# Kernel tuning notes

Hardware: AMD Instinct MI355X
Metric: run time of the kernel (lower is better)

The kernel has to match this reference:

```python
import jax, jax.numpy as jnp
import numpy as np
from jax import lax

ATT = 16
SK = 3
LK = 13
CIN = 64
RED = 2


def setup_inputs() -> dict:
    key = jax.random.key(0)
    ks = jax.random.split(key, 8)
    B, C, H, W = 16, CIN, 192, 192
    hid = ATT // RED
    x = jax.random.normal(ks[0], (B, C, H, W), dtype=jnp.float32)
    # kernel_gen: 1x1 convs on pooled features -> represented as dense matrices
    w1 = jax.random.normal(ks[1], (hid, ATT), dtype=jnp.float32) * (1.0 / np.sqrt(ATT))
    b1 = jnp.zeros((hid,), dtype=jnp.float32)
    # torch init zeros these; use small random values so the branch is exercised
    w2 = jax.random.normal(ks[2], (ATT * SK * SK, hid), dtype=jnp.float32) * 0.02
    b2 = jax.random.normal(ks[3], (ATT * SK * SK,), dtype=jnp.float32) * 0.02
    # kaiming fan_out for relu: std = sqrt(2 / (out_c * k * k))
    lk_std = np.sqrt(2.0 / (ATT * LK * LK))
    lk_filter = jax.random.normal(ks[4], (ATT, ATT, LK, LK), dtype=jnp.float32) * lk_std
    fusion_w = jax.random.normal(ks[5], (CIN, CIN), dtype=jnp.float32) * (1.0 / np.sqrt(CIN))
    fusion_b = jax.random.normal(ks[6], (CIN,), dtype=jnp.float32) * 0.01
    return {"x": x, "w1": w1, "b1": b1, "w2": w2, "b2": b2,
            "lk_filter": lk_filter, "fusion_w": fusion_w, "fusion_b": fusion_b}


def _forward(x, w1, b1, w2, b2, lk_filter, fusion_w, fusion_b):
    B, C, H, W = x.shape
    F_att, F_idt = x[:, :ATT], x[:, ATT:]

    # kernel_gen: global avg pool -> 1x1 conv -> GELU (exact) -> 1x1 conv
    pooled = F_att.mean(axis=(2, 3))                       # (B, ATT)
    h1 = jax.nn.gelu(pooled @ w1.T + b1, approximate=False)  # (B, ATT//RED)
    k = (h1 @ w2.T + b2).reshape(B, ATT, SK, SK)           # per-sample depthwise kernels

    # dynamic per-sample depthwise conv: 9-tap shifted multiply-accumulate
    pad = SK // 2
    xp = jnp.pad(F_att, ((0, 0), (0, 0), (pad, pad), (pad, pad)))
    out_dk = jnp.zeros_like(F_att)
    for i in range(SK):
        for j in range(SK):
            out_dk = out_dk + xp[:, :, i:i + H, j:j + W] * k[:, :, i, j][:, :, None, None]

    # dense large-kernel conv, padding 'same'
    lp = LK // 2
    out_lk = lax.conv_general_dilated(
        F_att, lk_filter, window_strides=(1, 1),
        padding=((lp, lp), (lp, lp)),
        dimension_numbers=("NCHW", "OIHW", "NCHW"))

    out = jnp.concatenate([out_lk + out_dk, F_idt], axis=1)  # (B, CIN, H, W)
    # fusion 1x1 conv
    out = jnp.einsum("bchw,oc->bohw", out, fusion_w) + fusion_b[None, :, None, None]
    return out


def reference(x, w1, b1, w2, b2, lk_filter, fusion_w, fusion_b):
    return _forward(x, w1, b1, w2, b2, lk_filter, fusion_w, fusion_b)
```

## Files before the change

kernel.cpp:

```cpp
#include <hip/hip_runtime.h>
#include <math.h>

#define ATT 16
#define SKK 3
#define LKK 13
#define CIN 64
#define HID 8
#define BB 16
#define HH 192
#define WW 192
#define HW (HH*WW)
#define NTAP 178
#define NPAIR 89

#define TH 16
#define TW 32
#define TILE_H (TH+12)
#define TILE_W (TW+12)
#define TILE_PX (TILE_H*TILE_W)
#define HSZ (TILE_PX*16)

#define FSTRIDE 144

typedef __attribute__((ext_vector_type(8))) short short8;
typedef __attribute__((ext_vector_type(4))) float f32x4;

__device__ inline unsigned short f2bf(float f) {
    unsigned u = __builtin_bit_cast(unsigned, f);
    unsigned r = u + 0x7FFFu + ((u >> 16) & 1u);
    return (unsigned short)(r >> 16);
}

__global__ __launch_bounds__(256) void pool_kernel(const float* __restrict__ x,
                                                   float* __restrict__ pooled) {
    int bc = blockIdx.x;
    int b = bc >> 4, c = bc & 15;
    const float4* p = (const float4*)(x + ((size_t)(b*CIN + c)) * HW);
    float s = 0.f;
    #pragma unroll 4
    for (int i = threadIdx.x; i < (HW/4); i += 256) {
        float4 v = p[i];
        s += (v.x + v.y) + (v.z + v.w);
    }
    #pragma unroll
    for (int off = 32; off > 0; off >>= 1) s += __shfl_down(s, off, 64);
    __shared__ float red[4];
    int lane = threadIdx.x & 63, wid = threadIdx.x >> 6;
    if (lane == 0) red[wid] = s;
    __syncthreads();
    if (threadIdx.x == 0)
        pooled[bc] = (red[0] + red[1] + red[2] + red[3]) * (1.0f/HW);
}

__global__ __launch_bounds__(256) void mlp_kernel(const float* __restrict__ pooled,
                                                  const float* __restrict__ w1,
                                                  const float* __restrict__ b1,
                                                  const float* __restrict__ w2,
                                                  const float* __restrict__ b2,
                                                  float* __restrict__ kout) {
    __shared__ float h1[BB][HID];
    int t = threadIdx.x;
    if (t < BB*HID) {
        int b = t / HID, j = t % HID;
        float s = b1[j];
        #pragma unroll
        for (int a = 0; a < ATT; ++a) s += pooled[b*ATT + a] * w1[j*ATT + a];
        h1[b][j] = 0.5f * s * (1.0f + erff(s * 0.70710678118654752440f));
    }
    __syncthreads();
    for (int idx = t; idx < BB*ATT*SKK*SKK; idx += 256) {
        int b = idx / (ATT*SKK*SKK), o = idx % (ATT*SKK*SKK);
        float s = b2[o];
        #pragma unroll
        for (int a = 0; a < HID; ++a) s += h1[b][a] * w2[o*HID + a];
        kout[idx] = s;
    }
}

__global__ __launch_bounds__(256) void build_kernel(const float* __restrict__ lk,
                                                    const float* __restrict__ kdyn,
                                                    const float* __restrict__ fw,
                                                    unsigned short* __restrict__ wB,
                                                    unsigned short* __restrict__ fwBt) {
    int idx = blockIdx.x*256 + threadIdx.x;
    const int total = BB*NTAP*256;
    if (idx < total) {
        int b   = idx / (NTAP*256);
        int rem = idx % (NTAP*256);
        int t   = rem >> 8;
        int co  = (rem >> 4) & 15;
        int ci  = rem & 15;
        float v;
        if (t < 169) v = lk[(co*ATT + ci)*169 + t];
        else { int d = t - 169; v = (ci == co) ? kdyn[(b*ATT + ci)*9 + d] : 0.f; }
        wB[idx] = f2bf(v);
    } else {
        int j = idx - total;
        if (j < CIN*CIN) fwBt[j] = f2bf(fw[j]);
    }
}

__global__ __launch_bounds__(256, 3) void conv_mfma_kernel(const float* __restrict__ x,
                                                           const unsigned short* __restrict__ wB,
                                                           float* __restrict__ convres) {
    __shared__ char ldsA[2*HSZ];
    __shared__ int  lut[NTAP];
    const int b    = blockIdx.y;
    const int tile = blockIdx.x;
    const int h0   = (tile / (WW/TW)) * TH;
    const int w0   = (tile % (WW/TW)) * TW;
    const int tid  = threadIdx.x;

    if (tid < NTAP) {
        int off;
        if (tid < 169) off = (tid/13)*TILE_W + (tid%13);
        else { int d = tid - 169; off = (5 + d/3)*TILE_W + (5 + d%3); }
        lut[tid] = off * 16;
    }

    const float* xb = x + (size_t)b*CIN*HW;
    #pragma unroll
    for (int c4 = 0; c4 < 8; ++c4) {
        const float* p0 = xb + (size_t)(2*c4)*HW;
        const float* p1 = p0 + HW;
        const int half = c4 >> 2, c2 = c4 & 3;
        for (int base = 0; base < TILE_PX; base += 256) {
            int px = base + tid;
            if (px < TILE_PX) {
                int tr = px / TILE_W, tc = px % TILE_W;
                int gh = h0 + tr - 6, gw = w0 + tc - 6;
                unsigned v = 0;
                if ((unsigned)gh < HH && (unsigned)gw < WW) {
                    int o = gh*WW + gw;
                    v = (unsigned)f2bf(p0[o]) | ((unsigned)f2bf(p1[o]) << 16);
                }
                *(unsigned*)&ldsA[half*HSZ + px*16 + c2*4] = v;
            }
        }
    }
    __syncthreads();

    const int lane = tid & 63, wv = tid >> 6;
    const int g = lane >> 4, r = lane & 15;
    const int halfoff = (g & 1) * HSZ;
    const int tl = g >> 1;

    int pixbase[8];
    #pragma unroll
    for (int mi = 0; mi < 8; ++mi) {
        int m = wv*8 + mi;
        int py = m >> 1, pxx = (m & 1) * 16;
        pixbase[mi] = (py*TILE_W + pxx + r) * 16 + halfoff;
    }

    const unsigned short* wbb = wB + (size_t)b*NTAP*256 + (lane & 15)*16 + (g & 1)*8;

    f32x4 acc[8];
    #pragma unroll
    for (int mi = 0; mi < 8; ++mi) acc[mi] = (f32x4){0.f,0.f,0.f,0.f};

    for (int pair = 0; pair < NPAIR; ++pair) {
        int t    = 2*pair + tl;
        int toff = lut[t];
        short8 bfrag = *(const short8*)&wbb[(size_t)t*256];
        #pragma unroll
        for (int mi = 0; mi < 8; ++mi) {
            short8 afrag = *(const short8*)&ldsA[pixbase[mi] + toff];
            acc[mi] = __builtin_amdgcn_mfma_f32_16x16x32_bf16(afrag, bfrag, acc[mi], 0, 0, 0);
        }
    }

    float* cr = convres + ((size_t)b*ATT + (lane & 15)) * HW;
    #pragma unroll
    for (int mi = 0; mi < 8; ++mi) {
        int m = wv*8 + mi;
        int py = m >> 1, pxx = (m & 1) * 16;
        *(f32x4*)&cr[(size_t)(h0 + py)*WW + w0 + pxx + g*4] = acc[mi];
    }
}

__global__ __launch_bounds__(256, 4) void fusion_kernel(const float* __restrict__ x,
                                                        const float* __restrict__ convres,
                                                        const unsigned short* __restrict__ fwBt,
                                                        const float* __restrict__ fb,
                                                        float* __restrict__ out) {
    __shared__ char fusA[256*FSTRIDE];
    const int b     = blockIdx.y;
    const int px0   = blockIdx.x * 256;
    const int tid   = threadIdx.x;

    #pragma unroll 4
    for (int c2 = 0; c2 < 32; ++c2) {
        int c = 2*c2;
        const float* p0 = (c < ATT) ? (convres + ((size_t)b*ATT + c)*HW)
                                    : (x + ((size_t)b*CIN + c)*HW);
        const float* p1 = p0 + HW;
        int o = px0 + tid;
        unsigned v = (unsigned)f2bf(p0[o]) | ((unsigned)f2bf(p1[o]) << 16);
        *(unsigned*)&fusA[tid*FSTRIDE + c2*4] = v;
    }
    __syncthreads();

    const int lane = tid & 63, wv = tid >> 6;
    const int g = lane >> 4, col = lane & 15;

    short8 bf[4][2];
    #pragma unroll
    for (int ot = 0; ot < 4; ++ot)
        #pragma unroll
        for (int kc = 0; kc < 2; ++kc)
            bf[ot][kc] = *(const short8*)&fwBt[(ot*16 + col)*CIN + kc*32 + g*8];

    #pragma unroll
    for (int mi = 0; mi < 4; ++mi) {
        int mpx = (wv*4 + mi) * 16;
        int apx = mpx + (lane & 15);
        short8 a0 = *(const short8*)&fusA[apx*FSTRIDE + (g*8)*2];
        short8 a1 = *(const short8*)&fusA[apx*FSTRIDE + (32 + g*8)*2];
        #pragma unroll
        for (int ot = 0; ot < 4; ++ot) {
            f32x4 acc = (f32x4){0.f,0.f,0.f,0.f};
            acc = __builtin_amdgcn_mfma_f32_16x16x32_bf16(a0, bf[ot][0], acc, 0, 0, 0);
            acc = __builtin_amdgcn_mfma_f32_16x16x32_bf16(a1, bf[ot][1], acc, 0, 0, 0);
            int o = ot*16 + col;
            f32x4 res = acc + fb[o];
            *(f32x4*)&out[((size_t)b*CIN + o)*HW + px0 + mpx + g*4] = res;
        }
    }
}

extern "C" void kernel_launch(void* const* d_in, const int* in_sizes, int n_in,
                              void* d_out, int out_size, void* d_ws, size_t ws_size,
                              hipStream_t stream) {
    const float* x   = (const float*)d_in[0];
    const float* w1  = (const float*)d_in[1];
    const float* b1  = (const float*)d_in[2];
    const float* w2  = (const float*)d_in[3];
    const float* b2  = (const float*)d_in[4];
    const float* lk  = (const float*)d_in[5];
    const float* fw  = (const float*)d_in[6];
    const float* fb  = (const float*)d_in[7];
    float* out = (float*)d_out;

    char* wsb = (char*)d_ws;
    float* pooled            = (float*)(wsb);
    float* kdyn              = (float*)(wsb + 1024);
    float* convres           = (float*)(wsb + 16384);
    unsigned short* wB       = (unsigned short*)(wsb + 16384 + (size_t)BB*ATT*HW*4);
    unsigned short* fwBt     = (unsigned short*)((char*)wB + (size_t)BB*NTAP*256*2);

    pool_kernel<<<dim3(BB*ATT), dim3(256), 0, stream>>>(x, pooled);
    mlp_kernel<<<dim3(1), dim3(256), 0, stream>>>(pooled, w1, b1, w2, b2, kdyn);
    build_kernel<<<dim3((BB*NTAP*256 + CIN*CIN + 255)/256), dim3(256), 0, stream>>>(
        lk, kdyn, fw, wB, fwBt);
    conv_mfma_kernel<<<dim3((HH/TH)*(WW/TW), BB), dim3(256), 0, stream>>>(x, wB, convres);
    fusion_kernel<<<dim3(HW/256, BB), dim3(256), 0, stream>>>(x, convres, fwBt, fb, out);
}
```

Measured before the change: 391.0 us.

## Fuse fusion GEMM into conv kernel and fold dynamic taps into center weights

Merges the 1x1 fusion conv into the large-kernel conv kernel. Conv accumulators are converted to bf16 in LDS alongside the identity channels, so the fp32 convres round trip through global memory goes away. The 3x3 dynamic depthwise kernel is added onto the central taps of the 13x13 filter, which cuts the tap count from 178 to 170 (one extra tap pair is padding). The MLP kernel is merged into build_kernel, and the B-fragment for the next tap is prefetched before the MFMAs for the current one. In exchange, the identity channels are loaded twice per block in two chunks, LDS is reused with extra barriers, and some per-thread MLP work is recomputed.

```diff
diff --git a/kernel.cpp b/kernel.cpp
--- a/kernel.cpp
+++ b/kernel.cpp
@@ -10,8 +10,8 @@
 #define HH 192
 #define WW 192
 #define HW (HH*WW)
-#define NTAP 178
-#define NPAIR 89
+#define NTAP 170
+#define NPAIR 85
 
 #define TH 16
 #define TW 32
@@ -20,7 +20,8 @@
 #define TILE_PX (TILE_H*TILE_W)
 #define HSZ (TILE_PX*16)
 
-#define FSTRIDE 144
+#define FSTRIDE 136
+#define NIDT (CIN-ATT)
 
 typedef __attribute__((ext_vector_type(8))) short short8;
 typedef __attribute__((ext_vector_type(4))) float f32x4;
@@ -52,57 +53,49 @@
         pooled[bc] = (red[0] + red[1] + red[2] + red[3]) * (1.0f/HW);
 }
 
-__global__ __launch_bounds__(256) void mlp_kernel(const float* __restrict__ pooled,
-                                                  const float* __restrict__ w1,
-                                                  const float* __restrict__ b1,
-                                                  const float* __restrict__ w2,
-                                                  const float* __restrict__ b2,
-                                                  float* __restrict__ kout) {
-    __shared__ float h1[BB][HID];
-    int t = threadIdx.x;
-    if (t < BB*HID) {
-        int b = t / HID, j = t % HID;
-        float s = b1[j];
-        #pragma unroll
-        for (int a = 0; a < ATT; ++a) s += pooled[b*ATT + a] * w1[j*ATT + a];
-        h1[b][j] = 0.5f * s * (1.0f + erff(s * 0.70710678118654752440f));
-    }
-    __syncthreads();
-    for (int idx = t; idx < BB*ATT*SKK*SKK; idx += 256) {
-        int b = idx / (ATT*SKK*SKK), o = idx % (ATT*SKK*SKK);
-        float s = b2[o];
-        #pragma unroll
-        for (int a = 0; a < HID; ++a) s += h1[b][a] * w2[o*HID + a];
-        kout[idx] = s;
-    }
-}
-
-__global__ __launch_bounds__(256) void build_kernel(const float* __restrict__ lk,
-                                                    const float* __restrict__ kdyn,
-                                                    const float* __restrict__ fw,
-                                                    unsigned short* __restrict__ wB,
-                                                    unsigned short* __restrict__ fwBt) {
-    int idx = blockIdx.x*256 + threadIdx.x;
-    const int total = BB*NTAP*256;
-    if (idx < total) {
-        int b   = idx / (NTAP*256);
-        int rem = idx % (NTAP*256);
-        int t   = rem >> 8;
-        int co  = (rem >> 4) & 15;
-        int ci  = rem & 15;
-        float v;
-        if (t < 169) v = lk[(co*ATT + ci)*169 + t];
-        else { int d = t - 169; v = (ci == co) ? kdyn[(b*ATT + ci)*9 + d] : 0.f; }
-        wB[idx] = f2bf(v);
+__global__ __launch_bounds__(256) void build_kernel(
+    const float* __restrict__ lk, const float* __restrict__ pooled,
+    const float* __restrict__ w1, const float* __restrict__ b1,
+    const float* __restrict__ w2, const float* __restrict__ b2,
+    const float* __restrict__ fw,
+    unsigned short* __restrict__ wB, unsigned short* __restrict__ fwBt)
+{
+    int blk = blockIdx.x;
+    if (blk < BB*NTAP) {
+        int b = blk / NTAP, t = blk % NTAP;
+        int co = threadIdx.x >> 4, ci = threadIdx.x & 15;
+        float v = 0.f;
+        if (t < 169) {
+            v = lk[(co*ATT + ci)*169 + t];
+            int ti = t / 13, tj = t % 13;
+            if (ti >= 5 && ti <= 7 && tj >= 5 && tj <= 7 && ci == co) {
+                float h[HID];
+                #pragma unroll
+                for (int a = 0; a < HID; ++a) {
+                    float s = b1[a];
+                    #pragma unroll
+                    for (int q = 0; q < ATT; ++q) s += pooled[b*ATT + q] * w1[a*ATT + q];
+                    h[a] = 0.5f * s * (1.0f + erff(s * 0.70710678118654752440f));
+                }
+                int o = ci*9 + (ti-5)*3 + (tj-5);
+                float s = b2[o];
+                #pragma unroll
+                for (int a = 0; a < HID; ++a) s += h[a] * w2[o*HID + a];
+                v += s;
+            }
+        }
+        wB[((size_t)b*NTAP + t)*256 + co*16 + ci] = f2bf(v);
     } else {
-        int j = idx - total;
-        if (j < CIN*CIN) fwBt[j] = f2bf(fw[j]);
-    }
-}
-
-__global__ __launch_bounds__(256, 3) void conv_mfma_kernel(const float* __restrict__ x,
-                                                           const unsigned short* __restrict__ wB,
-                                                           float* __restrict__ convres) {
+        int idx = (blk - BB*NTAP)*256 + threadIdx.x;
+        fwBt[idx] = f2bf(fw[idx]);
+    }
+}
+
+__global__ __launch_bounds__(256, 3) void conv_fused_kernel(
+    const float* __restrict__ x, const unsigned short* __restrict__ wB,
+    const unsigned short* __restrict__ fwBt, const float* __restrict__ fb,
+    float* __restrict__ out)
+{
     __shared__ char ldsA[2*HSZ];
     __shared__ int  lut[NTAP];
     const int b    = blockIdx.y;
@@ -111,12 +104,7 @@
     const int w0   = (tile % (WW/TW)) * TW;
     const int tid  = threadIdx.x;
 
-    if (tid < NTAP) {
-        int off;
-        if (tid < 169) off = (tid/13)*TILE_W + (tid%13);
-        else { int d = tid - 169; off = (5 + d/3)*TILE_W + (5 + d%3); }
-        lut[tid] = off * 16;
-    }
+    if (tid < NTAP) lut[tid] = (tid < 169) ? ((tid/13)*TILE_W + (tid%13))*16 : 0;
 
     const float* xb = x + (size_t)b*CIN*HW;
     #pragma unroll
@@ -153,78 +141,80 @@
         pixbase[mi] = (py*TILE_W + pxx + r) * 16 + halfoff;
     }
 
-    const unsigned short* wbb = wB + (size_t)b*NTAP*256 + (lane & 15)*16 + (g & 1)*8;
+    const unsigned short* wbb = wB + (size_t)b*NTAP*256 + r*16 + (g & 1)*8;
 
     f32x4 acc[8];
     #pragma unroll
     for (int mi = 0; mi < 8; ++mi) acc[mi] = (f32x4){0.f,0.f,0.f,0.f};
 
-    for (int pair = 0; pair < NPAIR; ++pair) {
-        int t    = 2*pair + tl;
-        int toff = lut[t];
-        short8 bfrag = *(const short8*)&wbb[(size_t)t*256];
+    int tcur = tl;
+    short8 bcur = *(const short8*)&wbb[(size_t)tcur*256];
+    int ocur = lut[tcur];
+    for (int pair = 0; pair < NPAIR-1; ++pair) {
+        int tn = 2*(pair+1) + tl;
+        short8 bn = *(const short8*)&wbb[(size_t)tn*256];
+        int on = lut[tn];
         #pragma unroll
         for (int mi = 0; mi < 8; ++mi) {
-            short8 afrag = *(const short8*)&ldsA[pixbase[mi] + toff];
-            acc[mi] = __builtin_amdgcn_mfma_f32_16x16x32_bf16(afrag, bfrag, acc[mi], 0, 0, 0);
-        }
-    }
-
-    float* cr = convres + ((size_t)b*ATT + (lane & 15)) * HW;
+            short8 af = *(const short8*)&ldsA[pixbase[mi] + ocur];
+            acc[mi] = __builtin_amdgcn_mfma_f32_16x16x32_bf16(af, bcur, acc[mi], 0, 0, 0);
+        }
+        bcur = bn; ocur = on;
+    }
     #pragma unroll
     for (int mi = 0; mi < 8; ++mi) {
-        int m = wv*8 + mi;
-        int py = m >> 1, pxx = (m & 1) * 16;
-        *(f32x4*)&cr[(size_t)(h0 + py)*WW + w0 + pxx + g*4] = acc[mi];
-    }
-}
-
-__global__ __launch_bounds__(256, 4) void fusion_kernel(const float* __restrict__ x,
-                                                        const float* __restrict__ convres,
-                                                        const unsigned short* __restrict__ fwBt,
-                                                        const float* __restrict__ fb,
-                                                        float* __restrict__ out) {
-    __shared__ char fusA[256*FSTRIDE];
-    const int b     = blockIdx.y;
-    const int px0   = blockIdx.x * 256;
-    const int tid   = threadIdx.x;
-
-    #pragma unroll 4
-    for (int c2 = 0; c2 < 32; ++c2) {
-        int c = 2*c2;
-        const float* p0 = (c < ATT) ? (convres + ((size_t)b*ATT + c)*HW)
-                                    : (x + ((size_t)b*CIN + c)*HW);
-        const float* p1 = p0 + HW;
-        int o = px0 + tid;
-        unsigned v = (unsigned)f2bf(p0[o]) | ((unsigned)f2bf(p1[o]) << 16);
-        *(unsigned*)&fusA[tid*FSTRIDE + c2*4] = v;
-    }
-    __syncthreads();
-
-    const int lane = tid & 63, wv = tid >> 6;
-    const int g = lane >> 4, col = lane & 15;
-
-    short8 bf[4][2];
+        short8 af = *(const short8*)&ldsA[pixbase[mi] + ocur];
+        acc[mi] = __builtin_amdgcn_mfma_f32_16x16x32_bf16(af, bcur, acc[mi], 0, 0, 0);
+    }
+
+    short8 bfw[4][2];
     #pragma unroll
     for (int ot = 0; ot < 4; ++ot)
         #pragma unroll
         for (int kc = 0; kc < 2; ++kc)
-            bf[ot][kc] = *(const short8*)&fwBt[(ot*16 + col)*CIN + kc*32 + g*8];
-
-    #pragma unroll
-    for (int mi = 0; mi < 4; ++mi) {
-        int mpx = (wv*4 + mi) * 16;
-        int apx = mpx + (lane & 15);
-        short8 a0 = *(const short8*)&fusA[apx*FSTRIDE + (g*8)*2];
-        short8 a1 = *(const short8*)&fusA[apx*FSTRIDE + (32 + g*8)*2];
+            bfw[ot][kc] = *(const short8*)&fwBt[(ot*16 + r)*CIN + kc*32 + g*8];
+    float fbv[4];
+    #pragma unroll
+    for (int ot = 0; ot < 4; ++ot) fbv[ot] = fb[ot*16 + r];
+
+    const int prow = tid >> 5, pcol = tid & 31;
+    for (int ck = 0; ck < 2; ++ck) {
+        __syncthreads();
+        size_t gbase = ((size_t)b*CIN + ATT)*HW + (size_t)(h0 + ck*8 + prow)*WW + w0 + pcol;
+        #pragma unroll 4
+        for (int c2 = 0; c2 < 24; ++c2) {
+            float v0 = x[gbase + (size_t)(2*c2)*HW];
+            float v1 = x[gbase + (size_t)(2*c2+1)*HW];
+            *(unsigned*)&ldsA[tid*FSTRIDE + 32 + c2*4] =
+                (unsigned)f2bf(v0) | ((unsigned)f2bf(v1) << 16);
+        }
+        if ((wv >> 1) == ck) {
+            #pragma unroll
+            for (int mi = 0; mi < 8; ++mi) {
+                int m = wv*8 + mi, py = m >> 1, pxx = (m & 1)*16;
+                int pl0 = (py - ck*8)*32 + pxx + g*4;
+                #pragma unroll
+                for (int j = 0; j < 4; ++j)
+                    *(unsigned short*)&ldsA[(pl0 + j)*FSTRIDE + r*2] = f2bf(acc[mi][j]);
+            }
+        }
+        __syncthreads();
         #pragma unroll
-        for (int ot = 0; ot < 4; ++ot) {
-            f32x4 acc = (f32x4){0.f,0.f,0.f,0.f};
-            acc = __builtin_amdgcn_mfma_f32_16x16x32_bf16(a0, bf[ot][0], acc, 0, 0, 0);
-            acc = __builtin_amdgcn_mfma_f32_16x16x32_bf16(a1, bf[ot][1], acc, 0, 0, 0);
-            int o = ot*16 + col;
-            f32x4 res = acc + fb[o];
-            *(f32x4*)&out[((size_t)b*CIN + o)*HW + px0 + mpx + g*4] = res;
+        for (int q = 0; q < 4; ++q) {
+            int mt = wv*4 + q;
+            int arow = mt*16 + r;
+            short8 a0 = *(const short8*)&ldsA[arow*FSTRIDE + g*16];
+            short8 a1 = *(const short8*)&ldsA[arow*FSTRIDE + 64 + g*16];
+            #pragma unroll
+            for (int ot = 0; ot < 4; ++ot) {
+                f32x4 ac = (f32x4){0.f,0.f,0.f,0.f};
+                ac = __builtin_amdgcn_mfma_f32_16x16x32_bf16(a0, bfw[ot][0], ac, 0, 0, 0);
+                ac = __builtin_amdgcn_mfma_f32_16x16x32_bf16(a1, bfw[ot][1], ac, 0, 0, 0);
+                ac = ac + fbv[ot];
+                int row = ck*8 + (mt >> 1), col = (mt & 1)*16 + g*4;
+                *(f32x4*)&out[((size_t)b*CIN + ot*16 + r)*HW
+                              + (size_t)(h0 + row)*WW + w0 + col] = ac;
+            }
         }
     }
 }
@@ -243,16 +233,13 @@
     float* out = (float*)d_out;
 
     char* wsb = (char*)d_ws;
-    float* pooled            = (float*)(wsb);
-    float* kdyn              = (float*)(wsb + 1024);
-    float* convres           = (float*)(wsb + 16384);
-    unsigned short* wB       = (unsigned short*)(wsb + 16384 + (size_t)BB*ATT*HW*4);
-    unsigned short* fwBt     = (unsigned short*)((char*)wB + (size_t)BB*NTAP*256*2);
+    float* pooled        = (float*)(wsb);
+    unsigned short* wB   = (unsigned short*)(wsb + 1024);
+    unsigned short* fwBt = (unsigned short*)(wsb + 1024 + (size_t)BB*NTAP*256*2);
 
     pool_kernel<<<dim3(BB*ATT), dim3(256), 0, stream>>>(x, pooled);
-    mlp_kernel<<<dim3(1), dim3(256), 0, stream>>>(pooled, w1, b1, w2, b2, kdyn);
-    build_kernel<<<dim3((BB*NTAP*256 + CIN*CIN + 255)/256), dim3(256), 0, stream>>>(
-        lk, kdyn, fw, wB, fwBt);
-    conv_mfma_kernel<<<dim3((HH/TH)*(WW/TW), BB), dim3(256), 0, stream>>>(x, wB, convres);
-    fusion_kernel<<<dim3(HW/256, BB), dim3(256), 0, stream>>>(x, convres, fwBt, fb, out);
-}
+    build_kernel<<<dim3(BB*NTAP + 16), dim3(256), 0, stream>>>(
+        lk, pooled, w1, b1, w2, b2, fw, wB, fwBt);
+    conv_fused_kernel<<<dim3((HH/TH)*(WW/TW), BB), dim3(256), 0, stream>>>(
+        x, wB, fwBt, fb, out);
+}
```

Result: faster. 347.0 us (-11.3%).
